# Performance work log

Hardware: AMD Instinct MI355X
Metric: run time of the kernel (lower is better)

Reference implementation:

```python
import jax, jax.numpy as jnp
import numpy as np

B, L, H, NL = 32, 1024, 4, 2
D_BERT, D_PHY, D_ACC = 1024, 7, 2
C_IN = D_BERT + D_PHY + D_ACC
D = 32
K = 20
N = B * L
E = N * K


def setup_inputs() -> dict:
    key = jax.random.key(0)
    ks = jax.random.split(key, 10)
    return {
        "protbert": jax.random.normal(ks[0], (B, 1, L, D_BERT), jnp.float32),
        "phychem": jax.random.normal(ks[1], (B, 1, L, D_PHY), jnp.float32),
        "resacc": jax.random.normal(ks[2], (B, 1, L, D_ACC), jnp.float32),
        "edge_feat": jax.random.normal(ks[3], (E, 2), jnp.float32),
        "src_idx": jax.random.randint(ks[4], (E,), 0, N, jnp.int32),
        "dst_idx": (jnp.arange(E, dtype=jnp.int32) % N),  # every node gets exactly K in-edges
        "conv_w": jax.random.normal(ks[5], (D, C_IN, 7), jnp.float32) * 0.02,
        "conv_b": jnp.zeros((D,), jnp.float32),
        "bn_gamma": jnp.ones((D,), jnp.float32),
        "bn_beta": jnp.zeros((D,), jnp.float32),
        "bn_mean": jnp.zeros((D,), jnp.float32),
        "bn_var": jnp.ones((D,), jnp.float32),
        "fc_w": jax.random.normal(ks[6], (NL, H, D, D), jnp.float32) * 0.1,
        "attn_w": jax.random.normal(ks[7], (NL, H, 2 * D + 2), jnp.float32) * 0.1,
        "fc_edge_w": jax.random.normal(ks[8], (NL, H, D, 2), jnp.float32) * 0.1,
        "fc_eatt_w": jax.random.normal(ks[9], (NL, H, 2, 2), jnp.float32) * 0.1,
    }


def _leaky(x):
    return jnp.where(x >= 0, x, 0.01 * x)


def _seg_softmax(e, dst, n):
    # softmax over incoming edges of each destination node (DGL mailbox softmax)
    m = jax.ops.segment_max(e, dst, num_segments=n)
    ex = jnp.exp(e - m[dst])
    s = jax.ops.segment_sum(ex, dst, num_segments=n)
    return ex / s[dst]


def reference(protbert, phychem, resacc, edge_feat, src_idx, dst_idx,
              conv_w, conv_b, bn_gamma, bn_beta, bn_mean, bn_var,
              fc_w, attn_w, fc_edge_w, fc_eatt_w):
    # --- Conv1d + LeakyReLU + BatchNorm1d (eval) encoder ---
    x = jnp.concatenate([protbert, phychem, resacc], axis=3)[:, 0]  # (B,L,C_IN)
    x = jnp.transpose(x, (0, 2, 1))  # (B,C_IN,L)
    x = jax.lax.conv_general_dilated(x, conv_w, (1,), [(3, 3)],
                                     dimension_numbers=("NCH", "OIH", "NCH"))
    x = _leaky(x + conv_b[None, :, None])
    scale = (bn_gamma / jnp.sqrt(bn_var + 1e-5))[None, :, None]
    x = (x - bn_mean[None, :, None]) * scale + bn_beta[None, :, None]
    feats = jnp.transpose(x, (0, 2, 1))  # (B,L,D)

    # --- stacked multi-head EGRET layers on flattened batched graph ---
    h = feats.reshape(N, D)
    alpha = None
    for l in range(NL):
        z = jnp.einsum("nd,hod->nho", h, fc_w[l])                    # (N,H,D)
        ex_t = jnp.einsum("ef,hgf->ehg", edge_feat, fc_eatt_w[l])    # (E,H,2) transformed edge feats for attn
        ez = jnp.einsum("ef,hof->eho", edge_feat, fc_edge_w[l])      # (E,H,D) edge messages
        a_src = attn_w[l][:, :D]
        a_dst = attn_w[l][:, D:2 * D]
        a_e = attn_w[l][:, 2 * D:]
        s_src = jnp.einsum("nhd,hd->nh", z, a_src)                   # node-level partial scores
        s_dst = jnp.einsum("nhd,hd->nh", z, a_dst)
        e = _leaky(s_src[src_idx] + s_dst[dst_idx]
                   + jnp.einsum("ehg,hg->eh", ex_t, a_e))            # (E,H)
        alpha = _seg_softmax(e, dst_idx, N)                          # (E,H)
        msg = alpha[:, :, None] * (z[src_idx] + ez)                  # attn on node+edge messages
        h = jax.ops.segment_sum(msg, dst_idx, num_segments=N).mean(axis=1)  # merge='avg'

    feats2 = h.reshape(B, L, D)
    out = jnp.concatenate([feats2, feats], axis=2)  # (B,L,2D)
    return out, alpha
```

## Files before the change

kernel.cpp:

```cpp
#include <hip/hip_runtime.h>
#include <hip/hip_bf16.h>
#include <cstdint>

#define B_   32
#define L_   1024
#define H_   4
#define NL_  2
#define D_   32
#define K_   20
#define N_   (B_ * L_)
#define E_   (N_ * K_)

typedef __attribute__((ext_vector_type(8))) __bf16 bf16x8;
typedef __attribute__((ext_vector_type(4))) float  f32x4;
typedef __attribute__((ext_vector_type(2))) float  f32x2;
typedef __attribute__((ext_vector_type(4))) int    i32x4;

static __device__ __forceinline__ float leaky1(float x) { return x >= 0.f ? x : 0.01f * x; }

static __device__ __forceinline__ bf16x8 cvt8(f32x4 lo, f32x4 hi) {
    bf16x8 r;
    r[0] = (__bf16)lo[0]; r[1] = (__bf16)lo[1]; r[2] = (__bf16)lo[2]; r[3] = (__bf16)lo[3];
    r[4] = (__bf16)hi[0]; r[5] = (__bf16)hi[1]; r[6] = (__bf16)hi[2]; r[7] = (__bf16)hi[3];
    return r;
}

__global__ __launch_bounds__(256) void k_prep_wbp(const float* __restrict__ conv_w,
                                                  __bf16* __restrict__ wbp) {
    int idx = blockIdx.x * 256 + threadIdx.x;
    if (idx >= 229376) return;
    int j    = idx & 7;
    int lane = (idx >> 3) & 63;
    int half = (idx >> 9) & 1;
    int cg   = (idx >> 10) & 31;
    int t    = idx >> 15;
    int d = half * 16 + (lane & 15);
    int c = cg * 32 + ((lane >> 4) << 3) + j;
    wbp[idx] = (__bf16)conv_w[d * 7231 + c * 7 + t];
}

static __device__ __forceinline__ void load_bfrag(const __bf16* __restrict__ wbp,
        int cg, int lane, bf16x8 (&br)[7][2]) {
    #pragma unroll
    for (int t = 0; t < 7; ++t) {
        const __bf16* wp = wbp + (size_t)(t * 32 + cg) * 1024 + lane * 8;
        br[t][0] = *(const bf16x8*)(wp);
        br[t][1] = *(const bf16x8*)(wp + 512);
    }
}

#define XRW4 70
__global__ __launch_bounds__(256) void k_conv_part(
    const float* __restrict__ protbert, const __bf16* __restrict__ wbp,
    __bf16* __restrict__ pbuf) {
    __shared__ __bf16 Xs[4 * 2 * (XRW4 * 32)];

    const int tid  = threadIdx.x;
    const int w    = tid >> 6;
    const int lane = tid & 63;
    const int tok0 = blockIdx.x * 256;
    const int b    = tok0 >> 10;
    const int lbw  = (tok0 & 1023) + w * 64;
    const int cb0  = blockIdx.y * 256;
    const int cg0  = blockIdx.y * 8;

    const float* agp[5];
    int aoffv[5];
    bool ex[5];
    #pragma unroll
    for (int q = 0; q < 5; ++q) {
        int u = lane + q * 64;
        bool e = (u < 280);
        int row = u >> 2, slot = u & 3;
        int l = lbw + row - 3;
        ex[q] = e;
        aoffv[q] = row * 32 + 8 * (slot ^ ((row >> 1) & 3));
        agp[q] = (e && (unsigned)l < 1024u)
            ? protbert + ((size_t)b * 1024 + l) * 1024 + cb0 + slot * 8 : nullptr;
    }
    __bf16* xw = &Xs[w * 2 * (XRW4 * 32)];

    const int row16 = lane & 15;
    const int kgrp  = lane >> 4;
    const int d0    = lane & 15;

    f32x4 acc[4][2];
    #pragma unroll
    for (int mt = 0; mt < 4; ++mt) {
        acc[mt][0] = (f32x4){0.f, 0.f, 0.f, 0.f};
        acc[mt][1] = (f32x4){0.f, 0.f, 0.f, 0.f};
    }

    bf16x8 brA[7][2], brB[7][2];

    {
        f32x4 pl[5], ph[5];
        #pragma unroll
        for (int q = 0; q < 5; ++q) {
            pl[q] = (f32x4){0,0,0,0}; ph[q] = (f32x4){0,0,0,0};
            if (agp[q]) { pl[q] = ((const f32x4*)agp[q])[0]; ph[q] = ((const f32x4*)agp[q])[1]; }
        }
        load_bfrag(wbp, cg0, lane, brA);
        #pragma unroll
        for (int q = 0; q < 5; ++q)
            if (ex[q]) *(bf16x8*)(&xw[aoffv[q]]) = cvt8(pl[q], ph[q]);
    }

    #pragma unroll
    for (int kk = 0; kk < 8; ++kk) {
        const int buf = kk & 1;
        const int xbase = buf * (XRW4 * 32);
        bf16x8 (&brCur)[7][2] = buf ? brB : brA;
        bf16x8 (&brNxt)[7][2] = buf ? brA : brB;
        f32x4 nl[5], nh[5];
        if (kk < 7) {
            #pragma unroll
            for (int q = 0; q < 5; ++q) {
                nl[q] = (f32x4){0,0,0,0}; nh[q] = (f32x4){0,0,0,0};
                if (agp[q]) {
                    nl[q] = ((const f32x4*)agp[q])[(kk + 1) * 8];
                    nh[q] = ((const f32x4*)agp[q])[(kk + 1) * 8 + 1];
                }
            }
            load_bfrag(wbp, cg0 + kk + 1, lane, brNxt);
        }
        #pragma unroll
        for (int t = 0; t < 7; ++t) {
            bf16x8 b0 = brCur[t][0];
            bf16x8 b1 = brCur[t][1];
            #pragma unroll
            for (int mt = 0; mt < 4; ++mt) {
                int arow = mt * 16 + row16 + t;
                bf16x8 a = *(const bf16x8*)(&xw[xbase + arow * 32 + 8 * (kgrp ^ ((arow >> 1) & 3))]);
                acc[mt][0] = __builtin_amdgcn_mfma_f32_16x16x32_bf16(a, b0, acc[mt][0], 0, 0, 0);
                acc[mt][1] = __builtin_amdgcn_mfma_f32_16x16x32_bf16(a, b1, acc[mt][1], 0, 0, 0);
            }
        }
        if (kk < 7) {
            const int nbase = (buf ^ 1) * (XRW4 * 32);
            #pragma unroll
            for (int q = 0; q < 5; ++q)
                if (ex[q]) *(bf16x8*)(&xw[nbase + aoffv[q]]) = cvt8(nl[q], nh[q]);
        }
    }

    __bf16* pb = pbuf + ((size_t)blockIdx.y * N_ + tok0) * 32;
    #pragma unroll
    for (int mt = 0; mt < 4; ++mt)
        #pragma unroll
        for (int i = 0; i < 4; ++i) {
            int lrow = w * 64 + mt * 16 + kgrp * 4 + i;
            pb[lrow * 32 + d0]      = (__bf16)acc[mt][0][i];
            pb[lrow * 32 + 16 + d0] = (__bf16)acc[mt][1][i];
        }
}

#define AROWS 70
__global__ __launch_bounds__(256) void k_epi_z0(
    const __bf16* __restrict__ pbuf,    const float* __restrict__ phychem,
    const float* __restrict__ resacc,   const float* __restrict__ conv_w,
    const float* __restrict__ conv_b,   const float* __restrict__ bn_gamma,
    const float* __restrict__ bn_beta,  const float* __restrict__ bn_mean,
    const float* __restrict__ bn_var,   const float* __restrict__ fc_w,
    const float* __restrict__ attn_w,
    float* __restrict__ out, __bf16* __restrict__ z,
    float* __restrict__ ssrc, float* __restrict__ sdst) {
    __shared__ float WT[4 * 1028];
    __shared__ float As[4 * 33], Ad[4 * 33];
    __shared__ float x9[AROWS * 9];
    __shared__ float w9[9 * 7 * 32];
    __shared__ float bnA[32], bnB[32], cb[32];
    __shared__ float fs[64 * 36];

    const int tid  = threadIdx.x;
    const int tok0 = blockIdx.x * 64;
    const int b    = tok0 >> 10;
    const int lb   = tok0 & 1023;

    for (int i = tid; i < 4096; i += 256) {
        int h = i >> 10, rem = i & 1023, o = rem >> 5, d = rem & 31;
        WT[h * 1028 + d * 32 + o] = fc_w[i];
    }
    {
        int h = tid >> 6, o = tid & 63;
        float v = attn_w[h * 66 + o];
        if (o < 32) As[h * 33 + o] = v; else Ad[h * 33 + (o - 32)] = v;
    }
    for (int i = tid; i < 9 * 7 * 32; i += 256) {
        int d = i & 31, jt = i >> 5, t = jt % 7, j = jt / 7;
        w9[i] = conv_w[d * 7231 + (1024 + j) * 7 + t];
    }
    for (int i = tid; i < AROWS * 9; i += 256) {
        int r = i / 9, j = i % 9;
        int l = lb + r - 3;
        float v = 0.f;
        if ((unsigned)l < 1024u)
            v = (j < 7) ? phychem[(b * 1024 + l) * 7 + j] : resacc[(b * 1024 + l) * 2 + (j - 7)];
        x9[i] = v;
    }
    if (tid < 32) {
        float sc = bn_gamma[tid] * rsqrtf(bn_var[tid] + 1e-5f);
        bnA[tid] = sc;
        bnB[tid] = bn_beta[tid] - bn_mean[tid] * sc;
        cb[tid]  = conv_b[tid];
    }
    __syncthreads();

    {
        const int d  = tid & 31;
        const int r0 = tid >> 5;
        #pragma unroll
        for (int q = 0; q < 8; ++q) {
            int lrow = r0 * 8 + q;
            int tok  = tok0 + lrow;
            float s = (float)pbuf[(size_t)tok * 32 + d]
                    + (float)pbuf[(size_t)(N_ + tok) * 32 + d]
                    + (float)pbuf[(size_t)(2 * N_ + tok) * 32 + d]
                    + (float)pbuf[(size_t)(3 * N_ + tok) * 32 + d];
            float c = 0.f;
            #pragma unroll
            for (int t = 0; t < 7; ++t) {
                const float* xr = &x9[(lrow + t) * 9];
                #pragma unroll
                for (int j = 0; j < 9; ++j) c += xr[j] * w9[(j * 7 + t) * 32 + d];
            }
            float v = leaky1(s + c + cb[d]) * bnA[d] + bnB[d];
            out[(size_t)tok * 64 + 32 + d] = v;
            fs[lrow * 36 + d] = v;
        }
    }
    __syncthreads();

    {
        const int nl = tid >> 2;
        const int h  = tid & 3;
        const int n  = tok0 + nl;

        float hrow[32];
        const f32x4* h4 = (const f32x4*)(&fs[nl * 36]);
        #pragma unroll
        for (int q = 0; q < 8; ++q) {
            f32x4 v = h4[q];
            hrow[q * 4 + 0] = v[0]; hrow[q * 4 + 1] = v[1];
            hrow[q * 4 + 2] = v[2]; hrow[q * 4 + 3] = v[3];
        }
        float zz[32];
        #pragma unroll
        for (int o = 0; o < 32; ++o) zz[o] = 0.f;
        #pragma unroll
        for (int d = 0; d < 32; ++d) {
            float hv = hrow[d];
            const f32x4* wt = (const f32x4*)&WT[h * 1028 + d * 32];
            #pragma unroll
            for (int o4 = 0; o4 < 8; ++o4) {
                f32x4 wv = wt[o4];
                zz[o4 * 4 + 0] += hv * wv[0]; zz[o4 * 4 + 1] += hv * wv[1];
                zz[o4 * 4 + 2] += hv * wv[2]; zz[o4 * 4 + 3] += hv * wv[3];
            }
        }
        float s1 = 0.f, s2 = 0.f;
        #pragma unroll
        for (int o = 0; o < 32; ++o) {
            s1 += zz[o] * As[h * 33 + o];
            s2 += zz[o] * Ad[h * 33 + o];
        }
        bf16x8* zo = (bf16x8*)(z + (size_t)n * 128 + h * 32);
        #pragma unroll
        for (int q = 0; q < 4; ++q) {
            bf16x8 v;
            #pragma unroll
            for (int j = 0; j < 8; ++j) v[j] = (__bf16)zz[q * 8 + j];
            zo[q] = v;
        }
        ssrc[n * 4 + h] = s1;
        sdst[n * 4 + h] = s2;
    }
}

__global__ __launch_bounds__(256) void k_z(
    const float* __restrict__ hin, const float* __restrict__ fc_w,
    const float* __restrict__ attn_w, int layer,
    __bf16* __restrict__ z, float* __restrict__ ssrc, float* __restrict__ sdst) {
    __shared__ float WT[4 * 1028];
    __shared__ float As[4 * 33], Ad[4 * 33];

    const int tid = threadIdx.x;
    for (int i = tid; i < 4096; i += 256) {
        int h = i >> 10, rem = i & 1023, o = rem >> 5, d = rem & 31;
        WT[h * 1028 + d * 32 + o] = fc_w[layer * 4096 + i];
    }
    {
        int h = tid >> 6, o = tid & 63;
        float v = attn_w[layer * (4 * 66) + h * 66 + o];
        if (o < 32) As[h * 33 + o] = v; else Ad[h * 33 + (o - 32)] = v;
    }
    __syncthreads();

    const int n = blockIdx.x * 64 + (tid >> 2);
    const int h = tid & 3;

    float hrow[32];
    const f32x4* h4 = (const f32x4*)(hin + (size_t)n * 32);
    #pragma unroll
    for (int q = 0; q < 8; ++q) {
        f32x4 v = h4[q];
        hrow[q * 4 + 0] = v[0]; hrow[q * 4 + 1] = v[1];
        hrow[q * 4 + 2] = v[2]; hrow[q * 4 + 3] = v[3];
    }

    float zz[32];
    #pragma unroll
    for (int o = 0; o < 32; ++o) zz[o] = 0.f;
    #pragma unroll
    for (int d = 0; d < 32; ++d) {
        float hv = hrow[d];
        const f32x4* wt = (const f32x4*)&WT[h * 1028 + d * 32];
        #pragma unroll
        for (int o4 = 0; o4 < 8; ++o4) {
            f32x4 wv = wt[o4];
            zz[o4 * 4 + 0] += hv * wv[0]; zz[o4 * 4 + 1] += hv * wv[1];
            zz[o4 * 4 + 2] += hv * wv[2]; zz[o4 * 4 + 3] += hv * wv[3];
        }
    }
    float s1 = 0.f, s2 = 0.f;
    #pragma unroll
    for (int o = 0; o < 32; ++o) {
        s1 += zz[o] * As[h * 33 + o];
        s2 += zz[o] * Ad[h * 33 + o];
    }
    bf16x8* zo = (bf16x8*)(z + (size_t)n * 128 + h * 32);
    #pragma unroll
    for (int q = 0; q < 4; ++q) {
        bf16x8 v;
        #pragma unroll
        for (int j = 0; j < 8; ++j) v[j] = (__bf16)zz[q * 8 + j];
        zo[q] = v;
    }
    ssrc[n * 4 + h] = s1;
    sdst[n * 4 + h] = s2;
}

__global__ __launch_bounds__(256) void k_node(
    const __bf16* __restrict__ z, const float* __restrict__ ssrc,
    const float* __restrict__ sdst, const int* __restrict__ src_idx,
    const float* __restrict__ edge_feat, const float* __restrict__ attn_w,
    const float* __restrict__ fc_edge_w, const float* __restrict__ fc_eatt_w,
    int layer, float* __restrict__ hout, int hout_stride,
    float* __restrict__ alpha_out) {
    __shared__ float sWe0[4 * 32], sWe1[4 * 32];
    __shared__ float sP[4][2];
    __shared__ float sAl[4][4][24];
    __shared__ float sF[4][4][2];
    __shared__ float sEf[4][20][2];
    __shared__ int   sS[4][24];

    const int tid = threadIdx.x;
    {
        int f = tid & 1, dd = (tid >> 1) & 31, h = tid >> 6;
        float v = fc_edge_w[layer * 256 + tid];
        if (f == 0) sWe0[h * 32 + dd] = v; else sWe1[h * 32 + dd] = v;
        if (tid < 8) {
            int hh = tid >> 1, ff = tid & 1;
            float ae0 = attn_w[layer * 264 + hh * 66 + 64];
            float ae1 = attn_w[layer * 264 + hh * 66 + 65];
            float w0  = fc_eatt_w[layer * 16 + hh * 4 + 0 + ff];
            float w1  = fc_eatt_w[layer * 16 + hh * 4 + 2 + ff];
            sP[hh][ff] = ae0 * w0 + ae1 * w1;
        }
    }
    const int slot = tid >> 6, tn = tid & 63;
    const int n = blockIdx.x * 4 + slot;
    __syncthreads();

    {
        int h = tn & 3;
        float sdv = sdst[n * 4 + h];
        #pragma unroll
        for (int p = 0; p < 2; ++p) {
            int k = p * 16 + (tn >> 2);
            if (p == 0 || tn < 16) {
                int e = n + k * N_;
                int s = src_idx[e];
                f32x2 ef = *(const f32x2*)(edge_feat + (size_t)e * 2);
                float sc = ssrc[s * 4 + h] + sdv + ef.x * sP[h][0] + ef.y * sP[h][1];
                sAl[slot][h][k] = leaky1(sc);
                if (h == 0) { sS[slot][k] = s; sEf[slot][k][0] = ef.x; sEf[slot][k][1] = ef.y; }
            }
        }
    }
    __syncthreads();

    if (tn < 4) {
        int h = tn;
        float m = -1e30f;
        for (int k = 0; k < 20; ++k) m = fmaxf(m, sAl[slot][h][k]);
        float ssum = 0.f;
        for (int k = 0; k < 20; ++k) {
            float v = __expf(sAl[slot][h][k] - m);
            sAl[slot][h][k] = v;
            ssum += v;
        }
        float inv = 1.f / ssum;
        float F0 = 0.f, F1 = 0.f;
        for (int k = 0; k < 20; ++k) {
            float a = sAl[slot][h][k] * inv;
            sAl[slot][h][k] = a;
            F0 += a * sEf[slot][k][0];
            F1 += a * sEf[slot][k][1];
        }
        sF[slot][h][0] = F0;
        sF[slot][h][1] = F1;
    }
    __syncthreads();

    if (alpha_out != nullptr) {
        #pragma unroll
        for (int p = 0; p < 2; ++p) {
            int k = p * 16 + (tn >> 2), h = tn & 3;
            if (p == 0 || tn < 16)
                alpha_out[(size_t)(n + k * N_) * 4 + h] = sAl[slot][h][k];
        }
    }

    {
        const int h = tn >> 4, dp = tn & 15;
        f32x4 areg[5];
        i32x4 sreg[5];
        #pragma unroll
        for (int q = 0; q < 5; ++q) {
            areg[q] = *(const f32x4*)(&sAl[slot][h][q * 4]);
            sreg[q] = *(const i32x4*)(&sS[slot][q * 4]);
        }
        float F0 = sF[slot][h][0], F1 = sF[slot][h][1];
        float w0a = sWe0[h * 32 + dp * 2], w0b = sWe0[h * 32 + dp * 2 + 1];
        float w1a = sWe1[h * 32 + dp * 2], w1b = sWe1[h * 32 + dp * 2 + 1];
        float acca = F0 * w0a + F1 * w1a;
        float accb = F0 * w0b + F1 * w1b;
        #pragma unroll
        for (int k = 0; k < 20; ++k) {
            int sk = __builtin_amdgcn_readfirstlane(sreg[k >> 2][k & 3]);
            const uint32_t* zp = (const uint32_t*)(z + (size_t)sk * 128);
            uint32_t u = zp[tn];
            float zl = __uint_as_float(u << 16);
            float zh = __uint_as_float(u & 0xffff0000u);
            float a = areg[k >> 2][k & 3];
            acca = fmaf(a, zl, acca);
            accb = fmaf(a, zh, accb);
        }
        acca += __shfl_xor(acca, 16); acca += __shfl_xor(acca, 32);
        accb += __shfl_xor(accb, 16); accb += __shfl_xor(accb, 32);
        if (tn < 16) {
            f32x2 o = {0.25f * acca, 0.25f * accb};
            *(f32x2*)(hout + (size_t)n * hout_stride + dp * 2) = o;
        }
    }
}

extern "C" void kernel_launch(void* const* d_in, const int* in_sizes, int n_in,
                              void* d_out, int out_size, void* d_ws, size_t ws_size,
                              hipStream_t stream) {
    const float* protbert  = (const float*)d_in[0];
    const float* phychem   = (const float*)d_in[1];
    const float* resacc    = (const float*)d_in[2];
    const float* edge_feat = (const float*)d_in[3];
    const int*   src_idx   = (const int*)d_in[4];
    const float* conv_w    = (const float*)d_in[6];
    const float* conv_b    = (const float*)d_in[7];
    const float* bn_gamma  = (const float*)d_in[8];
    const float* bn_beta   = (const float*)d_in[9];
    const float* bn_mean   = (const float*)d_in[10];
    const float* bn_var    = (const float*)d_in[11];
    const float* fc_w      = (const float*)d_in[12];
    const float* attn_w    = (const float*)d_in[13];
    const float* fc_edge_w = (const float*)d_in[14];
    const float* fc_eatt_w = (const float*)d_in[15];

    char* ws = (char*)d_ws;
    __bf16* wbp  = (__bf16*)(ws);
    float* h1    = (float*)(ws + (5u  << 20));
    float* ssrc  = (float*)(ws + (9u  << 20));
    float* sdst  = (float*)(ws + (10u << 20));
    __bf16* z    = (__bf16*)(ws + (11u << 20));
    __bf16* pbuf = (__bf16*)(ws + (24u << 20));

    float* out       = (float*)d_out;
    float* alpha_out = out + (size_t)N_ * 64;

    k_prep_wbp<<<896, 256, 0, stream>>>(conv_w, wbp);
    k_conv_part<<<dim3(128, 4), 256, 0, stream>>>(protbert, wbp, pbuf);
    k_epi_z0<<<512, 256, 0, stream>>>(pbuf, phychem, resacc, conv_w, conv_b,
                                      bn_gamma, bn_beta, bn_mean, bn_var,
                                      fc_w, attn_w, out, z, ssrc, sdst);
    k_node<<<N_ / 4, 256, 0, stream>>>(z, ssrc, sdst, src_idx, edge_feat, attn_w,
                                       fc_edge_w, fc_eatt_w, 0, h1, 32, nullptr);
    k_z<<<512, 256, 0, stream>>>(h1, fc_w, attn_w, 1, z, ssrc, sdst);
    k_node<<<N_ / 4, 256, 0, stream>>>(z, ssrc, sdst, src_idx, edge_feat, attn_w,
                                       fc_edge_w, fc_eatt_w, 1, out, 64, alpha_out);
}
```

Measured before the change: 135.0 us.

## Shrink conv tile to 16 tokens per wave and launch 4x more blocks

```diff
diff --git a/kernel.cpp b/kernel.cpp
--- a/kernel.cpp
+++ b/kernel.cpp
@@ -49,28 +49,28 @@
     }
 }
 
-#define XRW4 70
+#define XRW1 22
 __global__ __launch_bounds__(256) void k_conv_part(
     const float* __restrict__ protbert, const __bf16* __restrict__ wbp,
     __bf16* __restrict__ pbuf) {
-    __shared__ __bf16 Xs[4 * 2 * (XRW4 * 32)];
+    __shared__ __bf16 Xs[4 * 2 * (XRW1 * 32)];
 
     const int tid  = threadIdx.x;
     const int w    = tid >> 6;
     const int lane = tid & 63;
-    const int tok0 = blockIdx.x * 256;
+    const int tok0 = blockIdx.x * 64;
     const int b    = tok0 >> 10;
-    const int lbw  = (tok0 & 1023) + w * 64;
+    const int lbw  = (tok0 & 1023) + w * 16;
     const int cb0  = blockIdx.y * 256;
     const int cg0  = blockIdx.y * 8;
 
-    const float* agp[5];
-    int aoffv[5];
-    bool ex[5];
-    #pragma unroll
-    for (int q = 0; q < 5; ++q) {
+    const float* agp[2];
+    int aoffv[2];
+    bool ex[2];
+    #pragma unroll
+    for (int q = 0; q < 2; ++q) {
         int u = lane + q * 64;
-        bool e = (u < 280);
+        bool e = (u < 88);
         int row = u >> 2, slot = u & 3;
         int l = lbw + row - 3;
         ex[q] = e;
@@ -78,81 +78,66 @@
         agp[q] = (e && (unsigned)l < 1024u)
             ? protbert + ((size_t)b * 1024 + l) * 1024 + cb0 + slot * 8 : nullptr;
     }
-    __bf16* xw = &Xs[w * 2 * (XRW4 * 32)];
+    __bf16* xw = &Xs[w * 2 * (XRW1 * 32)];
 
     const int row16 = lane & 15;
     const int kgrp  = lane >> 4;
     const int d0    = lane & 15;
 
-    f32x4 acc[4][2];
-    #pragma unroll
-    for (int mt = 0; mt < 4; ++mt) {
-        acc[mt][0] = (f32x4){0.f, 0.f, 0.f, 0.f};
-        acc[mt][1] = (f32x4){0.f, 0.f, 0.f, 0.f};
-    }
-
-    bf16x8 brA[7][2], brB[7][2];
-
-    {
-        f32x4 pl[5], ph[5];
-        #pragma unroll
-        for (int q = 0; q < 5; ++q) {
+    f32x4 acc0 = {0.f, 0.f, 0.f, 0.f};
+    f32x4 acc1 = {0.f, 0.f, 0.f, 0.f};
+
+    {
+        f32x4 pl[2], ph[2];
+        #pragma unroll
+        for (int q = 0; q < 2; ++q) {
             pl[q] = (f32x4){0,0,0,0}; ph[q] = (f32x4){0,0,0,0};
             if (agp[q]) { pl[q] = ((const f32x4*)agp[q])[0]; ph[q] = ((const f32x4*)agp[q])[1]; }
         }
-        load_bfrag(wbp, cg0, lane, brA);
-        #pragma unroll
-        for (int q = 0; q < 5; ++q)
+        #pragma unroll
+        for (int q = 0; q < 2; ++q)
             if (ex[q]) *(bf16x8*)(&xw[aoffv[q]]) = cvt8(pl[q], ph[q]);
     }
 
     #pragma unroll
     for (int kk = 0; kk < 8; ++kk) {
         const int buf = kk & 1;
-        const int xbase = buf * (XRW4 * 32);
-        bf16x8 (&brCur)[7][2] = buf ? brB : brA;
-        bf16x8 (&brNxt)[7][2] = buf ? brA : brB;
-        f32x4 nl[5], nh[5];
+        const int xbase = buf * (XRW1 * 32);
+        bf16x8 br[7][2];
+        load_bfrag(wbp, cg0 + kk, lane, br);
+        f32x4 nl[2], nh[2];
         if (kk < 7) {
             #pragma unroll
-            for (int q = 0; q < 5; ++q) {
+            for (int q = 0; q < 2; ++q) {
                 nl[q] = (f32x4){0,0,0,0}; nh[q] = (f32x4){0,0,0,0};
                 if (agp[q]) {
                     nl[q] = ((const f32x4*)agp[q])[(kk + 1) * 8];
                     nh[q] = ((const f32x4*)agp[q])[(kk + 1) * 8 + 1];
                 }
             }
-            load_bfrag(wbp, cg0 + kk + 1, lane, brNxt);
         }
         #pragma unroll
         for (int t = 0; t < 7; ++t) {
-            bf16x8 b0 = brCur[t][0];
-            bf16x8 b1 = brCur[t][1];
+            int arow = row16 + t;
+            bf16x8 a = *(const bf16x8*)(&xw[xbase + arow * 32 + 8 * (kgrp ^ ((arow >> 1) & 3))]);
+            acc0 = __builtin_amdgcn_mfma_f32_16x16x32_bf16(a, br[t][0], acc0, 0, 0, 0);
+            acc1 = __builtin_amdgcn_mfma_f32_16x16x32_bf16(a, br[t][1], acc1, 0, 0, 0);
+        }
+        if (kk < 7) {
+            const int nbase = (buf ^ 1) * (XRW1 * 32);
             #pragma unroll
-            for (int mt = 0; mt < 4; ++mt) {
-                int arow = mt * 16 + row16 + t;
-                bf16x8 a = *(const bf16x8*)(&xw[xbase + arow * 32 + 8 * (kgrp ^ ((arow >> 1) & 3))]);
-                acc[mt][0] = __builtin_amdgcn_mfma_f32_16x16x32_bf16(a, b0, acc[mt][0], 0, 0, 0);
-                acc[mt][1] = __builtin_amdgcn_mfma_f32_16x16x32_bf16(a, b1, acc[mt][1], 0, 0, 0);
-            }
-        }
-        if (kk < 7) {
-            const int nbase = (buf ^ 1) * (XRW4 * 32);
-            #pragma unroll
-            for (int q = 0; q < 5; ++q)
+            for (int q = 0; q < 2; ++q)
                 if (ex[q]) *(bf16x8*)(&xw[nbase + aoffv[q]]) = cvt8(nl[q], nh[q]);
         }
     }
 
     __bf16* pb = pbuf + ((size_t)blockIdx.y * N_ + tok0) * 32;
     #pragma unroll
-    for (int mt = 0; mt < 4; ++mt)
-        #pragma unroll
-        for (int i = 0; i < 4; ++i) {
-            int lrow = w * 64 + mt * 16 + kgrp * 4 + i;
-            pb[lrow * 32 + d0]      = (__bf16)acc[mt][0][i];
-            pb[lrow * 32 + 16 + d0] = (__bf16)acc[mt][1][i];
-        }
+    for (int i = 0; i < 4; ++i) {
+        int lrow = w * 16 + kgrp * 4 + i;
+        pb[lrow * 32 + d0]      = (__bf16)acc0[i];
+        pb[lrow * 32 + 16 + d0] = (__bf16)acc1[i];
+    }
 }
 
 #define AROWS 70
@@ -487,7 +472,7 @@
     float* alpha_out = out + (size_t)N_ * 64;
 
     k_prep_wbp<<<896, 256, 0, stream>>>(conv_w, wbp);
-    k_conv_part<<<dim3(128, 4), 256, 0, stream>>>(protbert, wbp, pbuf);
+    k_conv_part<<<dim3(512, 4), 256, 0, stream>>>(protbert, wbp, pbuf);
     k_epi_z0<<<512, 256, 0, stream>>>(pbuf, phychem, resacc, conv_w, conv_b,
                                       bn_gamma, bn_beta, bn_mean, bn_var,
                                       fc_w, attn_w, out, z, ssrc, sdst);
```

Result: slower. 152.5 us (+13.0%).
